# Kernel tuning notes

Hardware: AMD Instinct MI355X
Metric: run time of the kernel (lower is better)

Reference implementation:

```python
import jax, jax.numpy as jnp
import numpy as np

N_NODES = 100000
N_EDGES = 800000
N_GRAPHS = 4000
EMB = 128      # node_emb_dims
HID = 256      # hidden_dims
FP = 2048      # fingerprint_dims
FIELD_DIMS = {"atom_type": 120, "degree": 12, "charge": 10}


def setup_inputs() -> dict:
    key = jax.random.key(0)
    ks = iter(jax.random.split(key, 40))
    p = lambda shape: jax.random.normal(next(ks), shape, dtype=jnp.float32) * 0.02
    inp = {
        "atom_idx": jax.random.randint(next(ks), (N_NODES,), 0, FIELD_DIMS["atom_type"]),
        "degree_idx": jax.random.randint(next(ks), (N_NODES,), 0, FIELD_DIMS["degree"]),
        "charge_idx": jax.random.randint(next(ks), (N_NODES,), 0, FIELD_DIMS["charge"]),
        "edge_index": jax.random.randint(next(ks), (2, N_EDGES), 0, N_NODES),
        "batch": jnp.sort(jax.random.randint(next(ks), (N_NODES,), 0, N_GRAPHS)),
        "fingerprint": jax.random.normal(next(ks), (N_GRAPHS, FP), dtype=jnp.float32),
        # FFM projector params
        "emb_atom": p((FIELD_DIMS["atom_type"], EMB)),
        "emb_degree": p((FIELD_DIMS["degree"], EMB)),
        "emb_charge": p((FIELD_DIMS["charge"], EMB)),
        "proj_w1": p((3 * EMB, EMB)), "proj_b1": jnp.zeros((EMB,), jnp.float32),
        "proj_w2": p((EMB, EMB)), "proj_b2": jnp.zeros((EMB,), jnp.float32),
        # fingerprint linear
        "fp_w": p((FP, HID)), "fp_b": jnp.zeros((HID,), jnp.float32),
        # GCN layers
        "conv_w0": p((EMB, HID)), "conv_b0": jnp.zeros((HID,), jnp.float32),
        "conv_w1": p((HID, HID)), "conv_b1": jnp.zeros((HID,), jnp.float32),
        "conv_w2": p((HID, HID)), "conv_b2": jnp.zeros((HID,), jnp.float32),
        "conv_w3": p((HID, HID)), "conv_b3": jnp.zeros((HID,), jnp.float32),
        # head
        "lin1_w": p((2 * HID, HID // 2)), "lin1_b": jnp.zeros((HID // 2,), jnp.float32),
        "lin2_w": p((HID // 2, 1)), "lin2_b": jnp.zeros((1,), jnp.float32),
    }
    return inp


def gcn_conv(x, w, b, src, dst, n):
    # PyG GCNConv: linear, add self-loops, symmetric norm, scatter-add at dst, + bias
    xw = x @ w
    loop = jnp.arange(n)
    src_f = jnp.concatenate([src, loop])
    dst_f = jnp.concatenate([dst, loop])
    deg = jax.ops.segment_sum(jnp.ones_like(dst_f, dtype=x.dtype), dst_f, num_segments=n)
    dinv = jax.lax.rsqrt(deg)  # deg >= 1 thanks to self-loops
    norm = dinv[src_f] * dinv[dst_f]                       # [E+N]
    msg = xw[src_f] * norm[:, None]                        # [E+N, HID]
    return jax.ops.segment_sum(msg, dst_f, num_segments=n) + b


def reference(atom_idx, degree_idx, charge_idx, edge_index, batch, fingerprint,
              emb_atom, emb_degree, emb_charge,
              proj_w1, proj_b1, proj_w2, proj_b2, fp_w, fp_b,
              conv_w0, conv_b0, conv_w1, conv_b1, conv_w2, conv_b2, conv_w3, conv_b3,
              lin1_w, lin1_b, lin2_w, lin2_b):
    # FieldAwareFactorizationMachine projector (vectorized over all nodes)
    e = jnp.concatenate([emb_atom[atom_idx], emb_degree[degree_idx], emb_charge[charge_idx]], axis=-1)
    h = jax.nn.relu(e @ proj_w1 + proj_b1) @ proj_w2 + proj_b2   # [N, EMB]
    src, dst = edge_index[0], edge_index[1]
    for w, b in ((conv_w0, conv_b0), (conv_w1, conv_b1), (conv_w2, conv_b2), (conv_w3, conv_b3)):
        h = jax.nn.relu(gcn_conv(h, w, b, src, dst, N_NODES))
    pooled = jax.ops.segment_sum(h, batch, num_segments=N_GRAPHS)  # scatter sum pooling
    fp_emb = fingerprint @ fp_w + fp_b
    z = jnp.concatenate([fp_emb, pooled], axis=-1)                 # [B, 2*HID]
    z = jax.nn.relu(z @ lin1_w + lin1_b)
    return z @ lin2_w + lin2_b                                     # [B, 1]
```

## Files before the change

### kernel.cpp

```cpp
#include <hip/hip_runtime.h>
#include <stdint.h>

#define NN 100000
#define NE 800000
#define NG 4000
#define NBLK ((NN + 255) / 256)

typedef __attribute__((ext_vector_type(8))) short s16x8;
typedef __attribute__((ext_vector_type(4))) float f32x4;
typedef __attribute__((ext_vector_type(2))) float f32x2;

__device__ __forceinline__ float b2f(unsigned short u) {
    return __uint_as_float(((unsigned int)u) << 16);
}
__device__ __forceinline__ unsigned short f2b(float f) {
    unsigned int x = __float_as_uint(f);
    x = x + 0x7FFFu + ((x >> 16) & 1u);
    return (unsigned short)(x >> 16);
}
__device__ __forceinline__ s16x8 cvt8(const float* __restrict__ p) {
    float4 a = *(const float4*)p;
    float4 b = *(const float4*)(p + 4);
    s16x8 r = {(short)f2b(a.x), (short)f2b(a.y), (short)f2b(a.z), (short)f2b(a.w),
               (short)f2b(b.x), (short)f2b(b.y), (short)f2b(b.z), (short)f2b(b.w)};
    return r;
}

__device__ __forceinline__ void gload16(const void* g, void* l) {
    __builtin_amdgcn_global_load_lds((const __attribute__((address_space(1))) unsigned int*)g,
                                     (__attribute__((address_space(3))) unsigned int*)l, 16, 0, 0);
}

__device__ __forceinline__ void acc8(f32x2* acc, s16x8 r) {
    const unsigned int* u = (const unsigned int*)&r;
#pragma unroll
    for (int q = 0; q < 4; ++q) {
        unsigned int w = u[q];
        f32x2 x;
        x[0] = __uint_as_float(w << 16);
        x[1] = __uint_as_float(w & 0xFFFF0000u);
        asm("v_pk_add_f32 %0, %1, %0" : "+v"(acc[q]) : "v"(x));
    }
}

__global__ void k_count(const int* __restrict__ dst, int* __restrict__ cnt) {
    int e = blockIdx.x * 256 + threadIdx.x;
    if (e < NE) atomicAdd(&cnt[dst[e]], 1);
}

__global__ __launch_bounds__(256) void k_bsum(const int* __restrict__ cnt, int* __restrict__ bsum) {
    __shared__ int s[256];
    int i = blockIdx.x * 256 + threadIdx.x;
    s[threadIdx.x] = (i < NN) ? cnt[i] : 0;
    __syncthreads();
    for (int off = 128; off; off >>= 1) {
        if (threadIdx.x < off) s[threadIdx.x] += s[threadIdx.x + off];
        __syncthreads();
    }
    if (threadIdx.x == 0) bsum[blockIdx.x] = s[0];
}

__global__ __launch_bounds__(512) void k_bscan(const int* __restrict__ bsum, int* __restrict__ bpre) {
    __shared__ int s[512];
    int t = threadIdx.x;
    int v = (t < NBLK) ? bsum[t] : 0;
    s[t] = v;
    __syncthreads();
    for (int off = 1; off < 512; off <<= 1) {
        int u = (t >= off) ? s[t - off] : 0;
        __syncthreads();
        s[t] += u;
        __syncthreads();
    }
    if (t < NBLK) bpre[t] = s[t] - v;
}

__global__ __launch_bounds__(256) void k_rowptr(const int* __restrict__ cnt, const int* __restrict__ bpre,
                                                int* __restrict__ row_ptr, int* __restrict__ cursor,
                                                float* __restrict__ dinv) {
    __shared__ int s[256];
    int t = threadIdx.x;
    int i = blockIdx.x * 256 + t;
    int v = (i < NN) ? cnt[i] : 0;
    s[t] = v;
    __syncthreads();
    for (int off = 1; off < 256; off <<= 1) {
        int u = (t >= off) ? s[t - off] : 0;
        __syncthreads();
        s[t] += u;
        __syncthreads();
    }
    if (i < NN) {
        int excl = bpre[blockIdx.x] + s[t] - v;
        row_ptr[i] = excl;
        cursor[i] = excl;
        dinv[i] = rsqrtf((float)(v + 1));
        if (i == NN - 1) row_ptr[NN] = NE;
    }
}

__global__ void k_fill(const int* __restrict__ src, const int* __restrict__ dst,
                       int* __restrict__ cursor, int* __restrict__ colA) {
    int e = blockIdx.x * 256 + threadIdx.x;
    if (e < NE) {
        int d = dst[e];
        int p = atomicAdd(&cursor[d], 1);
        colA[p] = src[e];
    }
}

struct TArgs {
    const float* src[7];
    unsigned short* dst[7];
    int kn[7];
    int ln[7];
    int off[8];
};

__global__ __launch_bounds__(256) void k_prep(TArgs a) {
    int i = blockIdx.x * 256 + threadIdx.x;
    if (i >= a.off[7]) return;
    int s = 0;
    while (i >= a.off[s + 1]) ++s;
    int j = i - a.off[s];
    int k = j >> a.ln[s], n = j & ((1 << a.ln[s]) - 1);
    a.dst[s][(size_t)n * (a.kn[s] >> a.ln[s]) + k] = f2b(a.src[s][j]);
}

__global__ void k_cvt(const float* __restrict__ src, unsigned short* __restrict__ dst, int n8) {
    int i = blockIdx.x * 256 + threadIdx.x;
    if (i < n8) *(s16x8*)&dst[(size_t)i * 8] = cvt8(&src[(size_t)i * 8]);
}

__global__ void k_binit(float* __restrict__ fe, const float* __restrict__ b) {
    int i = blockIdx.x * 256 + threadIdx.x;
    fe[i] = b[i & 255];
}

__global__ void k_z(const float* __restrict__ fe, unsigned short* __restrict__ zcat) {
    int i = blockIdx.x * 256 + threadIdx.x;
    int g = i >> 8, c = i & 255;
    zcat[(size_t)g * 512 + c] = f2b(fe[i]);
}

template <bool GATHER, bool BIAS, bool RELU, bool CBF16>
__global__ __launch_bounds__(256) void k_mm(
    const unsigned short* __restrict__ A, const unsigned short* __restrict__ Bt,
    void* __restrict__ Cv, const float* __restrict__ bias, int M, int N, int K,
    const int* __restrict__ ai, const int* __restrict__ di, const int* __restrict__ ci,
    const float* __restrict__ ea, const float* __restrict__ ed, const float* __restrict__ ec) {
    __shared__ unsigned short As[128 * 40];
    __shared__ unsigned short Bs[128 * 40];
    const int tid = threadIdx.x;
    const int row0 = blockIdx.x * 128, col0 = blockIdx.y * 128;
    const int lane = tid & 63, wid = tid >> 6;
    const int wrow = (wid >> 1) * 64, wcol = (wid & 1) * 64;
    const int lr = lane & 15, lk8 = (lane >> 4) * 8;

    const int sr = tid >> 1;
    const int skc = (tid & 1) * 16;
    const int agrow = row0 + sr;
    const int bgrow = col0 + sr;
    int ia = 0, idg = 0, ic = 0;
    if (GATHER && agrow < M) { ia = ai[agrow] * 128; idg = di[agrow] * 128; ic = ci[agrow] * 128; }

    f32x4 acc[4][4] = {};

    for (int kb = 0; kb < K; kb += 32) {
        if (kb) __syncthreads();
#pragma unroll
        for (int c = 0; c < 2; ++c) {
            int kloc = skc + c * 8;
            s16x8 v = {};
            if (agrow < M) {
                if (GATHER) {
                    int kg = kb + kloc;
                    const float* p = (kg < 128) ? (ea + ia + kg)
                                   : (kg < 256) ? (ed + idg + kg - 128)
                                                : (ec + ic + kg - 256);
                    v = cvt8(p);
                } else {
                    v = *(const s16x8*)&A[(size_t)agrow * K + kb + kloc];
                }
            }
            *(s16x8*)&As[sr * 40 + kloc] = v;
            s16x8 w = *(const s16x8*)&Bt[(size_t)bgrow * K + kb + kloc];
            *(s16x8*)&Bs[sr * 40 + kloc] = w;
        }
        __syncthreads();
        s16x8 af[4], bfr[4];
#pragma unroll
        for (int f = 0; f < 4; ++f)
            af[f] = *(const s16x8*)&As[(wrow + f * 16 + lr) * 40 + lk8];
#pragma unroll
        for (int f = 0; f < 4; ++f)
            bfr[f] = *(const s16x8*)&Bs[(wcol + f * 16 + lr) * 40 + lk8];
#pragma unroll
        for (int fm = 0; fm < 4; ++fm)
#pragma unroll
            for (int fn = 0; fn < 4; ++fn)
                acc[fm][fn] = __builtin_amdgcn_mfma_f32_16x16x32_bf16(af[fm], bfr[fn], acc[fm][fn], 0, 0, 0);
    }
#pragma unroll
    for (int fm = 0; fm < 4; ++fm) {
#pragma unroll
        for (int r = 0; r < 4; ++r) {
            int row = row0 + wrow + fm * 16 + (lane >> 4) * 4 + r;
            if (row < M) {
#pragma unroll
                for (int fn = 0; fn < 4; ++fn) {
                    int col = col0 + wcol + fn * 16 + lr;
                    float v = acc[fm][fn][r];
                    if (BIAS) v += bias[col];
                    if (RELU) v = fmaxf(v, 0.f);
                    if (CBF16) ((unsigned short*)Cv)[(size_t)row * N + col] = f2b(v);
                    else       ((float*)Cv)[(size_t)row * N + col] = v;
                }
            }
        }
    }
}

template <bool BIAS, bool RELU, bool CBF16, bool SPLITK, bool PRES>
__global__ __launch_bounds__(256) void k_mmA(
    const unsigned short* __restrict__ A, const unsigned short* __restrict__ Bt,
    void* __restrict__ Cv, const float* __restrict__ bias, const float* __restrict__ pres,
    int M, int N, int K, int kc) {
    __shared__ unsigned short As[2][128 * 32];
    __shared__ unsigned short Bs[2][128 * 32];
    const int tid = threadIdx.x;
    const int row0 = blockIdx.x * 128, col0 = blockIdx.y * 128;
    const int lane = tid & 63, wid = tid >> 6;
    const int wrow = (wid >> 1) * 64, wcol = (wid & 1) * 64;
    const int lr = lane & 15, lk8 = (lane >> 4) * 8;

    const int k0 = SPLITK ? blockIdx.z * kc : 0;
    const int nt = (SPLITK ? kc : K) / 32;

    const int sra = wid * 32 + (lane >> 2);
    const int sca = (lane & 3) * 8;
    const unsigned short* a0 = A + (size_t)min(row0 + sra, M - 1) * K + sca + k0;
    const unsigned short* a1 = A + (size_t)min(row0 + sra + 16, M - 1) * K + sca + k0;
    const unsigned short* b0 = Bt + (size_t)(col0 + sra) * K + sca + k0;
    const unsigned short* b1 = Bt + (size_t)(col0 + sra + 16) * K + sca + k0;
    const int lo0 = (wid * 2 + 0) * 512;
    const int lo1 = (wid * 2 + 1) * 512;

    f32x4 acc[4][4] = {};

    gload16(a0, &As[0][lo0]);
    gload16(a1, &As[0][lo1]);
    gload16(b0, &Bs[0][lo0]);
    gload16(b1, &Bs[0][lo1]);
    __syncthreads();

    int cur = 0;
    for (int t = 0; t < nt; ++t) {
        if (t + 1 < nt) {
            int kb = (t + 1) * 32;
            gload16(a0 + kb, &As[cur ^ 1][lo0]);
            gload16(a1 + kb, &As[cur ^ 1][lo1]);
            gload16(b0 + kb, &Bs[cur ^ 1][lo0]);
            gload16(b1 + kb, &Bs[cur ^ 1][lo1]);
        }
        s16x8 af[4], bfr[4];
#pragma unroll
        for (int f = 0; f < 4; ++f)
            af[f] = *(const s16x8*)&As[cur][(wrow + f * 16 + lr) * 32 + lk8];
#pragma unroll
        for (int f = 0; f < 4; ++f)
            bfr[f] = *(const s16x8*)&Bs[cur][(wcol + f * 16 + lr) * 32 + lk8];
#pragma unroll
        for (int fm = 0; fm < 4; ++fm)
#pragma unroll
            for (int fn = 0; fn < 4; ++fn)
                acc[fm][fn] = __builtin_amdgcn_mfma_f32_16x16x32_bf16(af[fm], bfr[fn], acc[fm][fn], 0, 0, 0);
        __syncthreads();
        cur ^= 1;
    }
#pragma unroll
    for (int fm = 0; fm < 4; ++fm) {
#pragma unroll
        for (int r = 0; r < 4; ++r) {
            int row = row0 + wrow + fm * 16 + (lane >> 4) * 4 + r;
            if (row < M) {
                float pr = PRES ? pres[row] : 1.f;
#pragma unroll
                for (int fn = 0; fn < 4; ++fn) {
                    int col = col0 + wcol + fn * 16 + lr;
                    float v = acc[fm][fn][r];
                    if (SPLITK) {
                        atomicAdd(&((float*)Cv)[(size_t)row * N + col], v);
                    } else {
                        if (BIAS) v += bias[col];
                        if (RELU) v = fmaxf(v, 0.f);
                        if (PRES) v *= pr;
                        if (CBF16) ((unsigned short*)Cv)[(size_t)row * N + col] = f2b(v);
                        else       ((float*)Cv)[(size_t)row * N + col] = v;
                    }
                }
            }
        }
    }
}

template <bool BIAS, bool RELU, bool CBF16, bool PRES>
__global__ __launch_bounds__(512) void k_mmB(
    const unsigned short* __restrict__ A, const unsigned short* __restrict__ Bt,
    void* __restrict__ Cv, const float* __restrict__ bias, const float* __restrict__ pres,
    int M, int K) {
    constexpr int N = 256;
    __shared__ unsigned short As[2][128 * 32];
    __shared__ unsigned short Bs[2][256 * 32];
    const int tid = threadIdx.x;
    const int row0 = blockIdx.x * 128;
    const int lane = tid & 63, wid = tid >> 6;
    const int wrow = (wid >> 2) * 64, wcol = (wid & 3) * 64;
    const int lr = lane & 15, lk8 = (lane >> 4) * 8;

    const int nt = K / 32;

    const int rsub = lane >> 2;
    const int csub = (lane & 3) * 8;
    const unsigned short* ga  = A  + (size_t)min(row0 + wid * 16 + rsub, M - 1) * K + csub;
    const unsigned short* gb0 = Bt + (size_t)(wid * 16 + rsub) * K + csub;
    const unsigned short* gb1 = Bt + (size_t)(128 + wid * 16 + rsub) * K + csub;
    const int la  = wid * 512;
    const int lb0 = wid * 512;
    const int lb1 = (8 + wid) * 512;

    f32x4 acc[4][4] = {};

    gload16(ga, &As[0][la]);
    gload16(gb0, &Bs[0][lb0]);
    gload16(gb1, &Bs[0][lb1]);
    __syncthreads();

    int cur = 0;
    for (int t = 0; t < nt; ++t) {
        if (t + 1 < nt) {
            int kb = (t + 1) * 32;
            gload16(ga + kb, &As[cur ^ 1][la]);
            gload16(gb0 + kb, &Bs[cur ^ 1][lb0]);
            gload16(gb1 + kb, &Bs[cur ^ 1][lb1]);
        }
        s16x8 af[4], bfr[4];
#pragma unroll
        for (int f = 0; f < 4; ++f)
            af[f] = *(const s16x8*)&As[cur][(wrow + f * 16 + lr) * 32 + lk8];
#pragma unroll
        for (int f = 0; f < 4; ++f)
            bfr[f] = *(const s16x8*)&Bs[cur][(wcol + f * 16 + lr) * 32 + lk8];
#pragma unroll
        for (int fm = 0; fm < 4; ++fm)
#pragma unroll
            for (int fn = 0; fn < 4; ++fn)
                acc[fm][fn] = __builtin_amdgcn_mfma_f32_16x16x32_bf16(af[fm], bfr[fn], acc[fm][fn], 0, 0, 0);
        __syncthreads();
        cur ^= 1;
    }
#pragma unroll
    for (int fm = 0; fm < 4; ++fm) {
#pragma unroll
        for (int r = 0; r < 4; ++r) {
            int row = row0 + wrow + fm * 16 + (lane >> 4) * 4 + r;
            if (row < M) {
                float pr = PRES ? pres[row] : 1.f;
#pragma unroll
                for (int fn = 0; fn < 4; ++fn) {
                    int col = wcol + fn * 16 + lr;
                    float v = acc[fm][fn][r];
                    if (BIAS) v += bias[col];
                    if (RELU) v = fmaxf(v, 0.f);
                    if (PRES) v *= pr;
                    if (CBF16) ((unsigned short*)Cv)[(size_t)row * N + col] = f2b(v);
                    else       ((float*)Cv)[(size_t)row * N + col] = v;
                }
            }
        }
    }
}

template <int WPN, bool FUSE>
__global__ __launch_bounds__(256) void k_scat3(const unsigned short* __restrict__ xw,
                                               unsigned short* __restrict__ hout,
                                               const float* __restrict__ dinv,
                                               const int* __restrict__ row_ptr,
                                               const int* __restrict__ colA,
                                               const float* __restrict__ bias) {
    constexpr int W = WPN * 128;
    constexpr int NPW = 4 / WPN;
    const int wid = threadIdx.x >> 6, lane = threadIdx.x & 63;
    const int grp = lane >> 4, li = lane & 15;
    const int v = (blockIdx.x * 4 + wid) * NPW + grp / WPN;
    const int cs = (WPN == 2) ? (grp & 1) * 128 : 0;
    const int c0 = cs + li * 8;

    const float dv = dinv[v];
    s16x8 rs = *(const s16x8*)&xw[(size_t)v * W + c0];

    f32x2 acc[4] = {};
    const int beg = row_ptr[v], end = row_ptr[v + 1];
    int p = beg;
    for (; p + 3 < end; p += 4) {
        int s0 = colA[p], s1 = colA[p + 1], s2 = colA[p + 2], s3 = colA[p + 3];
        s16x8 r0 = *(const s16x8*)&xw[(size_t)s0 * W + c0];
        s16x8 r1 = *(const s16x8*)&xw[(size_t)s1 * W + c0];
        s16x8 r2 = *(const s16x8*)&xw[(size_t)s2 * W + c0];
        s16x8 r3 = *(const s16x8*)&xw[(size_t)s3 * W + c0];
        acc8(acc, r0);
        acc8(acc, r1);
        acc8(acc, r2);
        acc8(acc, r3);
    }
    for (; p < end; ++p) {
        s16x8 r0 = *(const s16x8*)&xw[(size_t)colA[p] * W + c0];
        acc8(acc, r0);
    }

    unsigned short o[8];
#pragma unroll
    for (int j = 0; j < 8; ++j) {
        float a = acc[j >> 1][j & 1];
        a += b2f((unsigned short)rs[j]);
        a *= dv;
        if (FUSE) a = fmaxf(a + bias[c0 + j], 0.f);
        o[j] = f2b(a);
    }
    *(s16x8*)&hout[(size_t)v * W + c0] = *(const s16x8*)o;
}

__global__ void k_bounds(const int* __restrict__ batch, int* __restrict__ gstart) {
    int n = blockIdx.x * 256 + threadIdx.x;
    if (n >= NN) return;
    int b = batch[n];
    if (n == 0) {
        for (int g = 0; g <= b; ++g) gstart[g] = 0;
    } else {
        int pb = batch[n - 1];
        if (pb != b)
            for (int g = pb + 1; g <= b; ++g) gstart[g] = n;
    }
    if (n == NN - 1) {
        for (int g = b + 1; g <= NG; ++g) gstart[g] = NN;
    }
}

__global__ __launch_bounds__(64) void k_pool(const unsigned short* __restrict__ h,
                                             const int* __restrict__ gstart,
                                             unsigned short* __restrict__ zcat) {
    int g = blockIdx.x;
    int lane = threadIdx.x;
    int c0 = lane * 4;
    int beg = gstart[g], end = gstart[g + 1];
    float a0 = 0.f, a1 = 0.f, a2 = 0.f, a3 = 0.f;
    for (int n = beg; n < end; ++n) {
        ushort4 r = *(const ushort4*)&h[(size_t)n * 256 + c0];
        a0 += b2f(r.x); a1 += b2f(r.y); a2 += b2f(r.z); a3 += b2f(r.w);
    }
    ushort4 o;
    o.x = f2b(a0); o.y = f2b(a1); o.z = f2b(a2); o.w = f2b(a3);
    *(ushort4*)&zcat[(size_t)g * 512 + 256 + c0] = o;
}

__global__ __launch_bounds__(256) void k_dot(const float* __restrict__ z1,
                                             const float* __restrict__ w2,
                                             const float* __restrict__ b2,
                                             float* __restrict__ out) {
    int wid = threadIdx.x >> 6, lane = threadIdx.x & 63;
    int g = blockIdx.x * 4 + wid;
    float s = z1[(size_t)g * 128 + lane] * w2[lane]
            + z1[(size_t)g * 128 + 64 + lane] * w2[64 + lane];
#pragma unroll
    for (int off = 32; off; off >>= 1) s += __shfl_xor(s, off);
    if (lane == 0) out[g] = s + b2[0];
}

extern "C" void kernel_launch(void* const* d_in, const int* in_sizes, int n_in,
                              void* d_out, int out_size, void* d_ws, size_t ws_size,
                              hipStream_t stream) {
    const int* atom_idx   = (const int*)d_in[0];
    const int* degree_idx = (const int*)d_in[1];
    const int* charge_idx = (const int*)d_in[2];
    const int* edge_index = (const int*)d_in[3];
    const int* batch      = (const int*)d_in[4];
    const float* fingerprint = (const float*)d_in[5];
    const float* emb_atom   = (const float*)d_in[6];
    const float* emb_degree = (const float*)d_in[7];
    const float* emb_charge = (const float*)d_in[8];
    const float* proj_w1 = (const float*)d_in[9];
    const float* proj_b1 = (const float*)d_in[10];
    const float* proj_w2 = (const float*)d_in[11];
    const float* proj_b2 = (const float*)d_in[12];
    const float* fp_w = (const float*)d_in[13];
    const float* fp_b = (const float*)d_in[14];
    const float* conv_w[4] = {(const float*)d_in[15], (const float*)d_in[17],
                              (const float*)d_in[19], (const float*)d_in[21]};
    const float* conv_b[4] = {(const float*)d_in[16], (const float*)d_in[18],
                              (const float*)d_in[20], (const float*)d_in[22]};
    const float* lin1_w = (const float*)d_in[23];
    const float* lin1_b = (const float*)d_in[24];
    const float* lin2_w = (const float*)d_in[25];
    const float* lin2_b = (const float*)d_in[26];
    float* out = (float*)d_out;

    const int* src = edge_index;
    const int* dst = edge_index + NE;

    char* p = (char*)d_ws;
    auto carve = [&](size_t bytes) { void* r = (void*)p; p += (bytes + 255) & ~(size_t)255; return r; };
    unsigned short* bufA = (unsigned short*)carve((size_t)NN * 256 * 2);
    unsigned short* bufB = (unsigned short*)carve((size_t)NN * 256 * 2);
    int*   cnt     = (int*)carve((size_t)NN * 4);
    float* dinv    = (float*)carve((size_t)NN * 4);
    int*   row_ptr = (int*)carve((size_t)(NN + 1) * 4);
    int*   cursor  = (int*)carve((size_t)(NN + 1) * 4);
    int*   colA    = (int*)carve((size_t)NE * 4);
    int*   gstart  = (int*)carve((size_t)(NG + 1) * 4);
    float* fp_emb  = (float*)carve((size_t)NG * 256 * 4);
    int*   bsum    = (int*)carve((size_t)NBLK * 4);
    int*   bpre    = (int*)carve((size_t)NBLK * 4);
    unsigned short* w1t  = (unsigned short*)carve((size_t)128 * 384 * 2);
    unsigned short* w2t  = (unsigned short*)carve((size_t)128 * 128 * 2);
    unsigned short* cwt[4];
    cwt[0] = (unsigned short*)carve((size_t)256 * 128 * 2);
    for (int l = 1; l < 4; ++l) cwt[l] = (unsigned short*)carve((size_t)256 * 256 * 2);
    unsigned short* fpwt = (unsigned short*)carve((size_t)256 * 2048 * 2);
    unsigned short* fpbf = (unsigned short*)carve((size_t)NG * 2048 * 2);
    unsigned short* l1wt = (unsigned short*)carve((size_t)128 * 512 * 2);
    unsigned short* zcat = (unsigned short*)carve((size_t)NG * 512 * 2);
    float* z1      = (float*)carve((size_t)NG * 128 * 4);

    hipMemsetAsync(cnt, 0, (size_t)NN * 4, stream);
    k_count<<<(NE + 255) / 256, 256, 0, stream>>>(dst, cnt);
    k_bsum<<<NBLK, 256, 0, stream>>>(cnt, bsum);
    k_bscan<<<1, 512, 0, stream>>>(bsum, bpre);
    k_rowptr<<<NBLK, 256, 0, stream>>>(cnt, bpre, row_ptr, cursor, dinv);
    k_fill<<<(NE + 255) / 256, 256, 0, stream>>>(src, dst, cursor, colA);

    {
        TArgs a;
        const float* s7[7] = {proj_w1, proj_w2, conv_w[0], conv_w[1], conv_w[2], conv_w[3], fp_w};
        unsigned short* d7[7] = {w1t, w2t, cwt[0], cwt[1], cwt[2], cwt[3], fpwt};
        int kn7[7] = {49152, 16384, 32768, 65536, 65536, 65536, 524288};
        int ln7[7] = {7, 7, 8, 8, 8, 8, 8};
        int o = 0;
        for (int s = 0; s < 7; ++s) { a.src[s] = s7[s]; a.dst[s] = d7[s]; a.kn[s] = kn7[s]; a.ln[s] = ln7[s]; a.off[s] = o; o += kn7[s]; }
        a.off[7] = o;
        k_prep<<<(o + 255) / 256, 256, 0, stream>>>(a);
    }
    {
        TArgs a;
        a.src[0] = lin1_w; a.dst[0] = l1wt; a.kn[0] = 65536; a.ln[0] = 7; a.off[0] = 0;
        for (int s = 1; s < 7; ++s) { a.src[s] = lin1_w; a.dst[s] = l1wt; a.kn[s] = 0; a.ln[s] = 0; a.off[s] = 65536; }
        a.off[7] = 65536;
        k_prep<<<(65536 + 255) / 256, 256, 0, stream>>>(a);
    }
    k_cvt<<<(NG * 2048 / 8 + 255) / 256, 256, 0, stream>>>(fingerprint, fpbf, NG * 2048 / 8);

    k_binit<<<NG, 256, 0, stream>>>(fp_emb, fp_b);
    k_mmA<false, false, false, true, false><<<dim3((NG + 127) / 128, 2, 4), 256, 0, stream>>>(
        fpbf, fpwt, fp_emb, nullptr, nullptr, NG, 256, 2048, 512);
    k_z<<<NG, 256, 0, stream>>>(fp_emb, zcat);

    const int mg = (NN + 127) / 128;

    k_mm<true, true, true, true><<<dim3(mg, 1), 256, 0, stream>>>(
        nullptr, w1t, bufA, proj_b1, NN, 128, 384,
        atom_idx, degree_idx, charge_idx, emb_atom, emb_degree, emb_charge);
    k_mmA<true, false, true, false, true><<<dim3(mg, 1), 256, 0, stream>>>(
        bufA, w2t, bufB, proj_b2, dinv, NN, 128, 128, 0);

    k_scat3<1, false><<<NN / 16, 256, 0, stream>>>(bufB, bufA, dinv, row_ptr, colA, nullptr);
    k_mmB<true, true, true, false><<<mg, 512, 0, stream>>>(
        bufA, cwt[0], bufB, conv_b[0], nullptr, NN, 128);

    for (int l = 1; l < 4; ++l) {
        k_mmB<false, false, true, true><<<mg, 512, 0, stream>>>(
            bufB, cwt[l], bufA, nullptr, dinv, NN, 256);
        k_scat3<2, true><<<NN / 8, 256, 0, stream>>>(bufA, bufB, dinv, row_ptr, colA, conv_b[l]);
    }

    k_bounds<<<(NN + 255) / 256, 256, 0, stream>>>(batch, gstart);
    k_pool<<<NG, 64, 0, stream>>>(bufB, gstart, zcat);

    k_mmA<true, true, false, false, false><<<dim3((NG + 127) / 128, 1), 256, 0, stream>>>(
        zcat, l1wt, z1, lin1_b, nullptr, NG, 128, 512, 0);
    k_dot<<<NG / 4, 256, 0, stream>>>(z1, lin2_w, lin2_b, out);
}
```

Measured before the change: 709.5 us.

## Precompute embedding-projection tables and fold fingerprint linear into head weights

Because each node's first projection layer is linear in three small embedding lookups, per-row products emb@W1 are precomputed into a 142x128 table, and the per-node GEMM becomes a gather-and-add with bias and ReLU. The fingerprint linear is algebraically merged into lin1: fp_w is multiplied by the top half of lin1_w once, fp_b is folded into a new lin1 bias, and the head GEMM is split into a pooled part plus a split-K fingerprint part that accumulates into z1. ReLU moves into the final dot kernel. This removes the K=384 gather GEMM and the 4000x2048x256 fingerprint GEMM, at the cost of small precompute kernels and different rounding order.

```diff
diff --git a/kernel.cpp b/kernel.cpp
--- a/kernel.cpp
+++ b/kernel.cpp
@@ -132,93 +132,48 @@
     if (i < n8) *(s16x8*)&dst[(size_t)i * 8] = cvt8(&src[(size_t)i * 8]);
 }
 
-__global__ void k_binit(float* __restrict__ fe, const float* __restrict__ b) {
+__global__ __launch_bounds__(256) void k_tab(const float* __restrict__ ea, const float* __restrict__ ed,
+                                             const float* __restrict__ ec, const float* __restrict__ w1,
+                                             const float* __restrict__ fpb, const float* __restrict__ l1w,
+                                             const float* __restrict__ l1b,
+                                             float* __restrict__ Tcat, float* __restrict__ b1p) {
     int i = blockIdx.x * 256 + threadIdx.x;
-    fe[i] = b[i & 255];
-}
-
-__global__ void k_z(const float* __restrict__ fe, unsigned short* __restrict__ zcat) {
+    if (i < 142 * 128) {
+        int r = i >> 7, j = i & 127;
+        const float* src; int off, lr;
+        if (r < 120)      { src = ea; off = 0;   lr = r; }
+        else if (r < 132) { src = ed; off = 128; lr = r - 120; }
+        else              { src = ec; off = 256; lr = r - 132; }
+        float s = 0.f;
+        for (int k = 0; k < 128; ++k)
+            s = fmaf(src[lr * 128 + k], w1[(off + k) * 128 + j], s);
+        Tcat[i] = s;
+    } else if (i < 142 * 128 + 128) {
+        int j = i - 142 * 128;
+        float s = l1b[j];
+        for (int c = 0; c < 256; ++c)
+            s = fmaf(fpb[c], l1w[c * 128 + j], s);
+        b1p[j] = s;
+    }
+}
+
+__global__ __launch_bounds__(256) void k_emb(const int* __restrict__ ai, const int* __restrict__ di,
+                                             const int* __restrict__ ci, const float* __restrict__ Tcat,
+                                             const float* __restrict__ b1, unsigned short* __restrict__ h1) {
     int i = blockIdx.x * 256 + threadIdx.x;
-    int g = i >> 8, c = i & 255;
-    zcat[(size_t)g * 512 + c] = f2b(fe[i]);
-}
-
-template <bool GATHER, bool BIAS, bool RELU, bool CBF16>
-__global__ __launch_bounds__(256) void k_mm(
-    const unsigned short* __restrict__ A, const unsigned short* __restrict__ Bt,
-    void* __restrict__ Cv, const float* __restrict__ bias, int M, int N, int K,
-    const int* __restrict__ ai, const int* __restrict__ di, const int* __restrict__ ci,
-    const float* __restrict__ ea, const float* __restrict__ ed, const float* __restrict__ ec) {
-    __shared__ unsigned short As[128 * 40];
-    __shared__ unsigned short Bs[128 * 40];
-    const int tid = threadIdx.x;
-    const int row0 = blockIdx.x * 128, col0 = blockIdx.y * 128;
-    const int lane = tid & 63, wid = tid >> 6;
-    const int wrow = (wid >> 1) * 64, wcol = (wid & 1) * 64;
-    const int lr = lane & 15, lk8 = (lane >> 4) * 8;
-
-    const int sr = tid >> 1;
-    const int skc = (tid & 1) * 16;
-    const int agrow = row0 + sr;
-    const int bgrow = col0 + sr;
-    int ia = 0, idg = 0, ic = 0;
-    if (GATHER && agrow < M) { ia = ai[agrow] * 128; idg = di[agrow] * 128; ic = ci[agrow] * 128; }
-
-    f32x4 acc[4][4] = {};
-
-    for (int kb = 0; kb < K; kb += 32) {
-        if (kb) __syncthreads();
-#pragma unroll
-        for (int c = 0; c < 2; ++c) {
-            int kloc = skc + c * 8;
-            s16x8 v = {};
-            if (agrow < M) {
-                if (GATHER) {
-                    int kg = kb + kloc;
-                    const float* p = (kg < 128) ? (ea + ia + kg)
-                                   : (kg < 256) ? (ed + idg + kg - 128)
-                                                : (ec + ic + kg - 256);
-                    v = cvt8(p);
-                } else {
-                    v = *(const s16x8*)&A[(size_t)agrow * K + kb + kloc];
-                }
-            }
-            *(s16x8*)&As[sr * 40 + kloc] = v;
-            s16x8 w = *(const s16x8*)&Bt[(size_t)bgrow * K + kb + kloc];
-            *(s16x8*)&Bs[sr * 40 + kloc] = w;
-        }
-        __syncthreads();
-        s16x8 af[4], bfr[4];
-#pragma unroll
-        for (int f = 0; f < 4; ++f)
-            af[f] = *(const s16x8*)&As[(wrow + f * 16 + lr) * 40 + lk8];
-#pragma unroll
-        for (int f = 0; f < 4; ++f)
-            bfr[f] = *(const s16x8*)&Bs[(wcol + f * 16 + lr) * 40 + lk8];
-#pragma unroll
-        for (int fm = 0; fm < 4; ++fm)
-#pragma unroll
-            for (int fn = 0; fn < 4; ++fn)
-                acc[fm][fn] = __builtin_amdgcn_mfma_f32_16x16x32_bf16(af[fm], bfr[fn], acc[fm][fn], 0, 0, 0);
-    }
-#pragma unroll
-    for (int fm = 0; fm < 4; ++fm) {
-#pragma unroll
-        for (int r = 0; r < 4; ++r) {
-            int row = row0 + wrow + fm * 16 + (lane >> 4) * 4 + r;
-            if (row < M) {
-#pragma unroll
-                for (int fn = 0; fn < 4; ++fn) {
-                    int col = col0 + wcol + fn * 16 + lr;
-                    float v = acc[fm][fn][r];
-                    if (BIAS) v += bias[col];
-                    if (RELU) v = fmaxf(v, 0.f);
-                    if (CBF16) ((unsigned short*)Cv)[(size_t)row * N + col] = f2b(v);
-                    else       ((float*)Cv)[(size_t)row * N + col] = v;
-                }
-            }
-        }
-    }
+    if (i >= NN * 16) return;
+    int n = i >> 4, c8 = (i & 15) * 8;
+    int a = ai[n], d = di[n], c = ci[n];
+    const float* ta = Tcat + a * 128 + c8;
+    const float* td = Tcat + (120 + d) * 128 + c8;
+    const float* tc = Tcat + (132 + c) * 128 + c8;
+    unsigned short o[8];
+#pragma unroll
+    for (int j = 0; j < 8; ++j) {
+        float v = ta[j] + td[j] + tc[j] + b1[c8 + j];
+        o[j] = f2b(fmaxf(v, 0.f));
+    }
+    *(s16x8*)&h1[(size_t)n * 128 + c8] = *(const s16x8*)o;
 }
 
 template <bool BIAS, bool RELU, bool CBF16, bool SPLITK, bool PRES>
@@ -448,7 +403,7 @@
 
 __global__ __launch_bounds__(64) void k_pool(const unsigned short* __restrict__ h,
                                              const int* __restrict__ gstart,
-                                             unsigned short* __restrict__ zcat) {
+                                             unsigned short* __restrict__ pooled) {
     int g = blockIdx.x;
     int lane = threadIdx.x;
     int c0 = lane * 4;
@@ -460,7 +415,7 @@
     }
     ushort4 o;
     o.x = f2b(a0); o.y = f2b(a1); o.z = f2b(a2); o.w = f2b(a3);
-    *(ushort4*)&zcat[(size_t)g * 512 + 256 + c0] = o;
+    *(ushort4*)&pooled[(size_t)g * 256 + c0] = o;
 }
 
 __global__ __launch_bounds__(256) void k_dot(const float* __restrict__ z1,
@@ -469,8 +424,8 @@
                                              float* __restrict__ out) {
     int wid = threadIdx.x >> 6, lane = threadIdx.x & 63;
     int g = blockIdx.x * 4 + wid;
-    float s = z1[(size_t)g * 128 + lane] * w2[lane]
-            + z1[(size_t)g * 128 + 64 + lane] * w2[64 + lane];
+    float s = fmaxf(z1[(size_t)g * 128 + lane], 0.f) * w2[lane]
+            + fmaxf(z1[(size_t)g * 128 + 64 + lane], 0.f) * w2[64 + lane];
 #pragma unroll
     for (int off = 32; off; off >>= 1) s += __shfl_xor(s, off);
     if (lane == 0) out[g] = s + b2[0];
@@ -517,19 +472,21 @@
     int*   cursor  = (int*)carve((size_t)(NN + 1) * 4);
     int*   colA    = (int*)carve((size_t)NE * 4);
     int*   gstart  = (int*)carve((size_t)(NG + 1) * 4);
-    float* fp_emb  = (float*)carve((size_t)NG * 256 * 4);
     int*   bsum    = (int*)carve((size_t)NBLK * 4);
     int*   bpre    = (int*)carve((size_t)NBLK * 4);
-    unsigned short* w1t  = (unsigned short*)carve((size_t)128 * 384 * 2);
     unsigned short* w2t  = (unsigned short*)carve((size_t)128 * 128 * 2);
     unsigned short* cwt[4];
     cwt[0] = (unsigned short*)carve((size_t)256 * 128 * 2);
     for (int l = 1; l < 4; ++l) cwt[l] = (unsigned short*)carve((size_t)256 * 256 * 2);
-    unsigned short* fpwt = (unsigned short*)carve((size_t)256 * 2048 * 2);
-    unsigned short* fpbf = (unsigned short*)carve((size_t)NG * 2048 * 2);
-    unsigned short* l1wt = (unsigned short*)carve((size_t)128 * 512 * 2);
-    unsigned short* zcat = (unsigned short*)carve((size_t)NG * 512 * 2);
-    float* z1      = (float*)carve((size_t)NG * 128 * 4);
+    unsigned short* l1top = (unsigned short*)carve((size_t)128 * 256 * 2);
+    unsigned short* l1bot = (unsigned short*)carve((size_t)128 * 256 * 2);
+    unsigned short* fpwbf = (unsigned short*)carve((size_t)2048 * 256 * 2);
+    unsigned short* wfpt  = (unsigned short*)carve((size_t)128 * 2048 * 2);
+    unsigned short* fpbf  = (unsigned short*)carve((size_t)NG * 2048 * 2);
+    unsigned short* pooled = (unsigned short*)carve((size_t)NG * 256 * 2);
+    float* Tcat   = (float*)carve((size_t)142 * 128 * 4);
+    float* b1p    = (float*)carve((size_t)128 * 4);
+    float* z1     = (float*)carve((size_t)NG * 128 * 4);
 
     hipMemsetAsync(cnt, 0, (size_t)NN * 4, stream);
     k_count<<<(NE + 255) / 256, 256, 0, stream>>>(dst, cnt);
@@ -540,36 +497,31 @@
 
     {
         TArgs a;
-        const float* s7[7] = {proj_w1, proj_w2, conv_w[0], conv_w[1], conv_w[2], conv_w[3], fp_w};
-        unsigned short* d7[7] = {w1t, w2t, cwt[0], cwt[1], cwt[2], cwt[3], fpwt};
-        int kn7[7] = {49152, 16384, 32768, 65536, 65536, 65536, 524288};
-        int ln7[7] = {7, 7, 8, 8, 8, 8, 8};
+        const float* s7[7] = {proj_w2, conv_w[0], conv_w[1], conv_w[2], conv_w[3],
+                              lin1_w, lin1_w + 256 * 128};
+        unsigned short* d7[7] = {w2t, cwt[0], cwt[1], cwt[2], cwt[3], l1top, l1bot};
+        int kn7[7] = {16384, 32768, 65536, 65536, 65536, 32768, 32768};
+        int ln7[7] = {7, 8, 8, 8, 8, 7, 7};
         int o = 0;
         for (int s = 0; s < 7; ++s) { a.src[s] = s7[s]; a.dst[s] = d7[s]; a.kn[s] = kn7[s]; a.ln[s] = ln7[s]; a.off[s] = o; o += kn7[s]; }
         a.off[7] = o;
         k_prep<<<(o + 255) / 256, 256, 0, stream>>>(a);
     }
-    {
-        TArgs a;
-        a.src[0] = lin1_w; a.dst[0] = l1wt; a.kn[0] = 65536; a.ln[0] = 7; a.off[0] = 0;
-        for (int s = 1; s < 7; ++s) { a.src[s] = lin1_w; a.dst[s] = l1wt; a.kn[s] = 0; a.ln[s] = 0; a.off[s] = 65536; }
-        a.off[7] = 65536;
-        k_prep<<<(65536 + 255) / 256, 256, 0, stream>>>(a);
-    }
+    k_cvt<<<(2048 * 256 / 8 + 255) / 256, 256, 0, stream>>>(fp_w, fpwbf, 2048 * 256 / 8);
     k_cvt<<<(NG * 2048 / 8 + 255) / 256, 256, 0, stream>>>(fingerprint, fpbf, NG * 2048 / 8);
 
-    k_binit<<<NG, 256, 0, stream>>>(fp_emb, fp_b);
-    k_mmA<false, false, false, true, false><<<dim3((NG + 127) / 128, 2, 4), 256, 0, stream>>>(
-        fpbf, fpwt, fp_emb, nullptr, nullptr, NG, 256, 2048, 512);
-    k_z<<<NG, 256, 0, stream>>>(fp_emb, zcat);
+    k_tab<<<(142 * 128 + 128 + 255) / 256, 256, 0, stream>>>(
+        emb_atom, emb_degree, emb_charge, proj_w1, fp_b, lin1_w, lin1_b, Tcat, b1p);
+
+    k_mmA<false, false, true, false, false><<<dim3(1, 16), 256, 0, stream>>>(
+        l1top, fpwbf, wfpt, nullptr, nullptr, 128, 2048, 256, 0);
+
+    k_emb<<<(NN * 16 + 255) / 256, 256, 0, stream>>>(
+        atom_idx, degree_idx, charge_idx, Tcat, proj_b1, bufA);
+    k_mmA<true, false, true, false, true><<<dim3((NN + 127) / 128, 1), 256, 0, stream>>>(
+        bufA, w2t, bufB, proj_b2, dinv, NN, 128, 128, 0);
 
     const int mg = (NN + 127) / 128;
-
-    k_mm<true, true, true, true><<<dim3(mg, 1), 256, 0, stream>>>(
-        nullptr, w1t, bufA, proj_b1, NN, 128, 384,
-        atom_idx, degree_idx, charge_idx, emb_atom, emb_degree, emb_charge);
-    k_mmA<true, false, true, false, true><<<dim3(mg, 1), 256, 0, stream>>>(
-        bufA, w2t, bufB, proj_b2, dinv, NN, 128, 128, 0);
 
     k_scat3<1, false><<<NN / 16, 256, 0, stream>>>(bufB, bufA, dinv, row_ptr, colA, nullptr);
     k_mmB<true, true, true, false><<<mg, 512, 0, stream>>>(
@@ -582,9 +534,11 @@
     }
 
     k_bounds<<<(NN + 255) / 256, 256, 0, stream>>>(batch, gstart);
-    k_pool<<<NG, 64, 0, stream>>>(bufB, gstart, zcat);
-
-    k_mmA<true, true, false, false, false><<<dim3((NG + 127) / 128, 1), 256, 0, stream>>>(
-        zcat, l1wt, z1, lin1_b, nullptr, NG, 128, 512, 0);
+    k_pool<<<NG, 64, 0, stream>>>(bufB, gstart, pooled);
+
+    k_mmA<true, false, false, false, false><<<dim3((NG + 127) / 128, 1), 256, 0, stream>>>(
+        pooled, l1bot, z1, b1p, nullptr, NG, 128, 256, 0);
+    k_mmA<false, false, false, true, false><<<dim3((NG + 127) / 128, 1, 4), 256, 0, stream>>>(
+        fpbf, wfpt, z1, nullptr, nullptr, NG, 128, 2048, 512);
     k_dot<<<NG / 4, 256, 0, stream>>>(z1, lin2_w, lin2_b, out);
 }
```

Result: faster. 681.4 us (-4.0%).
